# Performance work log

Hardware: AMD Instinct MI355X
Metric: run time of the kernel (lower is better)

## Reference

```python
import jax, jax.numpy as jnp
import numpy as np

N_NODES = 50000
N_EDGES = 800000
IN, HID, OUT = 128, 128, 64


def gcn_layer(x, W, b, src, dst, n):
    """PyG GCNConv: add self-loops, symmetric normalization, linear, scatter-add, bias."""
    loop = jnp.arange(n, dtype=src.dtype)
    s = jnp.concatenate([src, loop])  # message sources
    d = jnp.concatenate([dst, loop])  # message destinations
    deg = jax.ops.segment_sum(jnp.ones(s.shape[0], dtype=x.dtype), d, num_segments=n)
    dinv = jnp.where(deg > 0, jax.lax.rsqrt(deg), jnp.zeros_like(deg))
    norm = dinv[s] * dinv[d]  # [E+N]
    h = x @ W                 # dense transform first (PyG order)
    agg = jax.ops.segment_sum(h[s] * norm[:, None], d, num_segments=n)  # [N, out]
    return agg + b


def setup_inputs() -> dict:
    key = jax.random.key(0)
    ks = jax.random.split(key, 8)
    x = jax.random.normal(ks[0], (N_NODES, IN), dtype=jnp.float32)
    edge_index = jax.random.randint(ks[1], (2, N_EDGES), 0, N_NODES, dtype=jnp.int32)
    s = 0.05
    W1 = jax.random.normal(ks[2], (IN, HID), dtype=jnp.float32) * s
    b1 = jnp.zeros((HID,), dtype=jnp.float32)
    W2 = jax.random.normal(ks[3], (HID, HID), dtype=jnp.float32) * s
    b2 = jnp.zeros((HID,), dtype=jnp.float32)
    W3 = jax.random.normal(ks[4], (HID, OUT), dtype=jnp.float32) * s
    b3 = jnp.zeros((OUT,), dtype=jnp.float32)
    return {"x": x, "edge_index": edge_index, "W1": W1, "b1": b1,
            "W2": W2, "b2": b2, "W3": W3, "b3": b3}


def reference(x, edge_index, W1, b1, W2, b2, W3, b3):
    src, dst = edge_index[0], edge_index[1]
    n = x.shape[0]
    # dropout is identity in eval mode; ReLU follows every layer (incl. last) as in source
    h = jax.nn.relu(gcn_layer(x, W1, b1, src, dst, n))
    h = jax.nn.relu(gcn_layer(h, W2, b2, src, dst, n))
    h = jax.nn.relu(gcn_layer(h, W3, b3, src, dst, n))
    return jax.nn.log_softmax(h, axis=1)
```

## Files before the change

### kernel.cpp

```cpp
#include <hip/hip_runtime.h>
#include <math.h>


typedef __attribute__((ext_vector_type(8))) short short8;
typedef __attribute__((ext_vector_type(4))) float f32x4;

#define PADROW 50115
#define CAP 64
#define NPART 8

__device__ inline unsigned short f2bf(float x) {
    unsigned int u = __float_as_uint(x);
    u += 0x7fffu + ((u >> 16) & 1u);
    return (unsigned short)(u >> 16);
}
__device__ inline float blo(unsigned int v) { return __uint_as_float(v << 16); }
__device__ inline float bhi(unsigned int v) { return __uint_as_float(v & 0xffff0000u); }


__global__ void prep0_kernel(int* __restrict__ deg, int N,
                             unsigned int* __restrict__ col32, int colw,
                             const float* __restrict__ W1, unsigned short* __restrict__ W1t,
                             const float* __restrict__ W2, unsigned short* __restrict__ W2t,
                             const float* __restrict__ W3, unsigned short* __restrict__ W3t,
                             unsigned short* __restrict__ hbuf) {
    int i = blockIdx.x * blockDim.x + threadIdx.x;
    if (i < N) deg[i] = 0;
    if (i < colw) col32[i] = 0xC3C3C3C3u;
    if (i < 16384) {
        int k = i >> 7, n = i & 127;
        W1t[(size_t)n * 128 + k] = f2bf(W1[i]);
    } else if (i < 32768) {
        int j = i - 16384;
        int k = j >> 7, n = j & 127;
        W2t[(size_t)n * 128 + k] = f2bf(W2[j]);
    } else if (i < 40960) {
        int j = i - 32768;
        int k = j >> 6, n = j & 63;
        W3t[(size_t)n * 128 + k] = f2bf(W3[j]);
    }
    if (i < 16)
        ((uint4*)(hbuf + (size_t)PADROW * 128))[i] = make_uint4(0, 0, 0, 0);
}

__global__ void build_ell_kernel(const int* __restrict__ src, const int* __restrict__ dst,
                                 int* __restrict__ deg, unsigned short* __restrict__ col_ell,
                                 int E, int N, int nblk_per_part) {
    int part = blockIdx.x & (NPART - 1);
    int blk  = blockIdx.x / NPART;
    int npr = (N + NPART - 1) / NPART;
    int lo = part * npr;
    int hi = min(N, lo + npr);
    int stride = nblk_per_part * blockDim.x;
    for (int e = blk * blockDim.x + threadIdx.x; e < E; e += stride) {
        int d = dst[e];
        if (d >= lo && d < hi) {
            int rk = atomicAdd(&deg[d], 1);
            if (rk < CAP) col_ell[(size_t)d * CAP + rk] = (unsigned short)src[e];
        }
    }
}

template<int H, bool AF32>
__global__ __launch_bounds__(256) void gemm_mfma(const void* __restrict__ Av,
                                                 const unsigned short* __restrict__ Wt,
                                                 const int* __restrict__ deg,
                                                 unsigned short* __restrict__ C, int M) {
    __shared__ __attribute__((aligned(16))) unsigned short As[128][136];
    __shared__ __attribute__((aligned(16))) unsigned short Ws[H][136];
    int tid = threadIdx.x;
    int row0 = blockIdx.x * 128;
    if (AF32) {
        const float* A = (const float*)Av;
        #pragma unroll
        for (int g = tid; g < 128 * 32; g += 256) {
            int r = g >> 5, c = g & 31;
            int gr = row0 + r;
            ushort4 o = make_ushort4(0, 0, 0, 0);
            if (gr < M) {
                float4 v = *(const float4*)(A + (size_t)gr * 128 + c * 4);
                o.x = f2bf(v.x); o.y = f2bf(v.y); o.z = f2bf(v.z); o.w = f2bf(v.w);
            }
            *(ushort4*)&As[r][c * 4] = o;
        }
    } else {
        const unsigned short* A = (const unsigned short*)Av;
        #pragma unroll
        for (int g = tid; g < 128 * 16; g += 256) {
            int r = g >> 4, c = g & 15;
            int gr = row0 + r;
            uint4 v = make_uint4(0, 0, 0, 0);
            if (gr < M) v = *(const uint4*)(A + (size_t)gr * 128 + c * 8);
            *(uint4*)&As[r][c * 8] = v;
        }
    }
    #pragma unroll
    for (int g = tid; g < H * 16; g += 256) {
        int r = g >> 4, c = g & 15;
        *(uint4*)&Ws[r][c * 8] = *(const uint4*)(Wt + (size_t)r * 128 + c * 8);
    }
    if (H == 64 && blockIdx.x == 0 && tid < 8)
        ((uint4*)(C + (size_t)PADROW * 64))[tid] = make_uint4(0, 0, 0, 0);
    __syncthreads();

    int wave = tid >> 6, lane = tid & 63;
    int lr = lane & 15;
    int lk = (lane >> 4) * 8;

    short8 af[2][4];
    float dv[2][4];
    #pragma unroll
    for (int t = 0; t < 2; ++t) {
        int base = wave * 32 + t * 16;
        #pragma unroll
        for (int ks = 0; ks < 4; ++ks)
            af[t][ks] = *(const short8*)&As[base + lr][ks * 32 + lk];
        #pragma unroll
        for (int r = 0; r < 4; ++r) {
            int grow = row0 + base + (lane >> 4) * 4 + r;
            dv[t][r] = (grow < M) ? rsqrtf((float)deg[grow] + 1.0f) : 0.0f;
        }
    }

    #pragma unroll
    for (int ct = 0; ct < H / 16; ++ct) {
        f32x4 acc0 = {0.f, 0.f, 0.f, 0.f};
        f32x4 acc1 = {0.f, 0.f, 0.f, 0.f};
        #pragma unroll
        for (int ks = 0; ks < 4; ++ks) {
            short8 wf = *(const short8*)&Ws[ct * 16 + lr][ks * 32 + lk];
            acc0 = __builtin_amdgcn_mfma_f32_16x16x32_bf16(af[0][ks], wf, acc0, 0, 0, 0);
            acc1 = __builtin_amdgcn_mfma_f32_16x16x32_bf16(af[1][ks], wf, acc1, 0, 0, 0);
        }
        int gcol = ct * 16 + lr;
        #pragma unroll
        for (int r = 0; r < 4; ++r) {
            int g0 = row0 + wave * 32 + (lane >> 4) * 4 + r;
            if (g0 < M) C[(size_t)g0 * H + gcol] = f2bf(acc0[r] * dv[0][r]);
            int g1 = g0 + 16;
            if (g1 < M) C[(size_t)g1 * H + gcol] = f2bf(acc1[r] * dv[1][r]);
        }
    }
}

__global__ __launch_bounds__(256, 4) void spmm128_kernel(const uint2* __restrict__ h2,
                                                         const unsigned short* __restrict__ col_ell,
                                                         const int* __restrict__ deg,
                                                         const float* __restrict__ bias,
                                                         uint2* __restrict__ out2, int N) {
    int wid = blockIdx.x * 8 + (threadIdx.x >> 5);
    int c = threadIdx.x & 31;
    if (wid >= N) return;
    const uint4* cell4 = (const uint4*)(col_ell + (size_t)wid * CAP);
    int dg = deg[wid];
    uint2 hv = h2[(size_t)wid * 32 + c];
    float a0 = blo(hv.x), a1 = bhi(hv.x), a2 = blo(hv.y), a3 = bhi(hv.y);
    {
        uint4 q0 = cell4[0], q1 = cell4[1], q2 = cell4[2];
        unsigned int cw[12] = {q0.x, q0.y, q0.z, q0.w, q1.x, q1.y, q1.z, q1.w,
                               q2.x, q2.y, q2.z, q2.w};
        uint2 g[24];
        #pragma unroll
        for (int u = 0; u < 12; ++u) {
            g[2 * u]     = h2[(size_t)(cw[u] & 0xffffu) * 32 + c];
            g[2 * u + 1] = h2[(size_t)(cw[u] >> 16) * 32 + c];
        }
        #pragma unroll
        for (int u = 0; u < 24; ++u) {
            a0 += blo(g[u].x); a1 += bhi(g[u].x);
            a2 += blo(g[u].y); a3 += bhi(g[u].y);
        }
    }
    if (dg > 24) {
        uint4 q0 = cell4[3], q1 = cell4[4], q2 = cell4[5];
        unsigned int cw[12] = {q0.x, q0.y, q0.z, q0.w, q1.x, q1.y, q1.z, q1.w,
                               q2.x, q2.y, q2.z, q2.w};
        uint2 g[24];
        #pragma unroll
        for (int u = 0; u < 12; ++u) {
            g[2 * u]     = h2[(size_t)(cw[u] & 0xffffu) * 32 + c];
            g[2 * u + 1] = h2[(size_t)(cw[u] >> 16) * 32 + c];
        }
        #pragma unroll
        for (int u = 0; u < 24; ++u) {
            a0 += blo(g[u].x); a1 += bhi(g[u].x);
            a2 += blo(g[u].y); a3 += bhi(g[u].y);
        }
        if (dg > 48) {
            uint4 q0 = cell4[6], q1 = cell4[7];
            unsigned int cw[8] = {q0.x, q0.y, q0.z, q0.w, q1.x, q1.y, q1.z, q1.w};
            uint2 g[16];
            #pragma unroll
            for (int u = 0; u < 8; ++u) {
                g[2 * u]     = h2[(size_t)(cw[u] & 0xffffu) * 32 + c];
                g[2 * u + 1] = h2[(size_t)(cw[u] >> 16) * 32 + c];
            }
            #pragma unroll
            for (int u = 0; u < 16; ++u) {
                a0 += blo(g[u].x); a1 += bhi(g[u].x);
                a2 += blo(g[u].y); a3 += bhi(g[u].y);
            }
        }
    }
    float dv = rsqrtf((float)dg + 1.0f);
    float4 b4 = ((const float4*)bias)[c];
    a0 = fmaxf(fmaf(a0, dv, b4.x), 0.0f);
    a1 = fmaxf(fmaf(a1, dv, b4.y), 0.0f);
    a2 = fmaxf(fmaf(a2, dv, b4.z), 0.0f);
    a3 = fmaxf(fmaf(a3, dv, b4.w), 0.0f);
    uint2 o;
    o.x = (unsigned int)f2bf(a0) | ((unsigned int)f2bf(a1) << 16);
    o.y = (unsigned int)f2bf(a2) | ((unsigned int)f2bf(a3) << 16);
    out2[(size_t)wid * 32 + c] = o;
}

__global__ __launch_bounds__(256, 4) void spmm64_lsm_kernel(const unsigned int* __restrict__ h1,
                                                            const unsigned short* __restrict__ col_ell,
                                                            const int* __restrict__ deg,
                                                            const float* __restrict__ bias,
                                                            float2* __restrict__ out2, int N) {
    int wid = blockIdx.x * 8 + (threadIdx.x >> 5);
    int c = threadIdx.x & 31;
    if (wid >= N) return;
    const uint4* cell4 = (const uint4*)(col_ell + (size_t)wid * CAP);
    int dg = deg[wid];
    unsigned int hv = h1[(size_t)wid * 32 + c];
    float a0 = blo(hv), a1 = bhi(hv);
    {
        uint4 q0 = cell4[0], q1 = cell4[1], q2 = cell4[2];
        unsigned int cw[12] = {q0.x, q0.y, q0.z, q0.w, q1.x, q1.y, q1.z, q1.w,
                               q2.x, q2.y, q2.z, q2.w};
        unsigned int g[24];
        #pragma unroll
        for (int u = 0; u < 12; ++u) {
            g[2 * u]     = h1[(size_t)(cw[u] & 0xffffu) * 32 + c];
            g[2 * u + 1] = h1[(size_t)(cw[u] >> 16) * 32 + c];
        }
        #pragma unroll
        for (int u = 0; u < 24; ++u) { a0 += blo(g[u]); a1 += bhi(g[u]); }
    }
    if (dg > 24) {
        uint4 q0 = cell4[3], q1 = cell4[4], q2 = cell4[5];
        unsigned int cw[12] = {q0.x, q0.y, q0.z, q0.w, q1.x, q1.y, q1.z, q1.w,
                               q2.x, q2.y, q2.z, q2.w};
        unsigned int g[24];
        #pragma unroll
        for (int u = 0; u < 12; ++u) {
            g[2 * u]     = h1[(size_t)(cw[u] & 0xffffu) * 32 + c];
            g[2 * u + 1] = h1[(size_t)(cw[u] >> 16) * 32 + c];
        }
        #pragma unroll
        for (int u = 0; u < 24; ++u) { a0 += blo(g[u]); a1 += bhi(g[u]); }
        if (dg > 48) {
            uint4 q0 = cell4[6], q1 = cell4[7];
            unsigned int cw[8] = {q0.x, q0.y, q0.z, q0.w, q1.x, q1.y, q1.z, q1.w};
            unsigned int g[16];
            #pragma unroll
            for (int u = 0; u < 8; ++u) {
                g[2 * u]     = h1[(size_t)(cw[u] & 0xffffu) * 32 + c];
                g[2 * u + 1] = h1[(size_t)(cw[u] >> 16) * 32 + c];
            }
            #pragma unroll
            for (int u = 0; u < 16; ++u) { a0 += blo(g[u]); a1 += bhi(g[u]); }
        }
    }
    float dv = rsqrtf((float)dg + 1.0f);
    float2 b2 = ((const float2*)bias)[c];
    a0 = fmaxf(fmaf(a0, dv, b2.x), 0.0f);
    a1 = fmaxf(fmaf(a1, dv, b2.y), 0.0f);
    float m = fmaxf(a0, a1);
    #pragma unroll
    for (int off = 16; off; off >>= 1) m = fmaxf(m, __shfl_xor(m, off));
    float ssum = expf(a0 - m) + expf(a1 - m);
    #pragma unroll
    for (int off = 16; off; off >>= 1) ssum += __shfl_xor(ssum, off);
    float lse = m + logf(ssum);
    float2 o;
    o.x = a0 - lse;
    o.y = a1 - lse;
    out2[(size_t)wid * 32 + c] = o;
}


extern "C" void kernel_launch(void* const* d_in, const int* in_sizes, int n_in,
                              void* d_out, int out_size, void* d_ws, size_t ws_size,
                              hipStream_t stream) {
    const float* x  = (const float*)d_in[0];
    const int*   ei = (const int*)d_in[1];
    const float* W1 = (const float*)d_in[2];
    const float* b1 = (const float*)d_in[3];
    const float* W2 = (const float*)d_in[4];
    const float* b2 = (const float*)d_in[5];
    const float* W3 = (const float*)d_in[6];
    const float* b3 = (const float*)d_in[7];
    float* out = (float*)d_out;

    const int IN = 128, HID = 128, OUT = 64;
    int N = in_sizes[0] / IN;
    int E = in_sizes[1] / 2;
    const int* srcp = ei;
    const int* dstp = ei + E;

    char* p = (char*)d_ws;
    auto alloc = [&](size_t bytes) {
        char* r = p;
        p += (bytes + 255) & ~(size_t)255;
        return r;
    };
    int* deg = (int*)alloc((size_t)N * 4);
    unsigned short* col_ell = (unsigned short*)alloc((size_t)N * CAP * 2);
    unsigned short* W1t  = (unsigned short*)alloc((size_t)IN * HID * 2);
    unsigned short* W2t  = (unsigned short*)alloc((size_t)HID * HID * 2);
    unsigned short* W3t  = (unsigned short*)alloc((size_t)HID * OUT * 2);
    unsigned short* hbuf = (unsigned short*)alloc((size_t)(PADROW + 1) * HID * 2);
    unsigned short* abuf = (unsigned short*)alloc((size_t)N * HID * 2);

    int colw = N * CAP / 2;
    int prep0_grid = (max(colw, 40960) + 255) / 256;
    prep0_kernel<<<prep0_grid, 256, 0, stream>>>(deg, N, (unsigned int*)col_ell, colw,
                                                 W1, W1t, W2, W2t, W3, W3t, hbuf);
    int nblk_per_part = 512;
    build_ell_kernel<<<NPART * nblk_per_part, 256, 0, stream>>>(srcp, dstp, deg, col_ell,
                                                                E, N, nblk_per_part);

    int spmm_blocks = (N + 7) / 8;
    int gemm_blocks = (N + 127) / 128;

    gemm_mfma<128, true><<<gemm_blocks, 256, 0, stream>>>(x, W1t, deg, hbuf, N);
    spmm128_kernel<<<spmm_blocks, 256, 0, stream>>>((const uint2*)hbuf, col_ell, deg,
                                                    b1, (uint2*)abuf, N);
    gemm_mfma<128, false><<<gemm_blocks, 256, 0, stream>>>(abuf, W2t, deg, hbuf, N);
    spmm128_kernel<<<spmm_blocks, 256, 0, stream>>>((const uint2*)hbuf, col_ell, deg,
                                                    b2, (uint2*)abuf, N);
    gemm_mfma<64, false><<<gemm_blocks, 256, 0, stream>>>(abuf, W3t, deg, hbuf, N);
    spmm64_lsm_kernel<<<spmm_blocks, 256, 0, stream>>>((const unsigned int*)hbuf, col_ell, deg,
                                                       b3, (float2*)out, N);
}
```

Measured before the change: 161.9 us.

## Store 128-wide hidden features in column slices for cache-local SpMM gathers

Changes the 128-wide hidden buffers from row-major to eight 16-column slices, each laid out as [node][16]. GEMM outputs and inputs are rewritten to match, and a new SpMM kernel handles one slice per block, with 8 lanes per node and a degree-bounded loop. Each slice (~1.6MB) can stay in cache while its neighbour rows are gathered at random, which targets gather misses. In exchange it makes 8x more passes over the ELL index reads, issues narrower 4-byte gathers, and the strided GEMM stores and loads may coalesce less well.

```diff
diff --git a/kernel.cpp b/kernel.cpp
--- a/kernel.cpp
+++ b/kernel.cpp
@@ -6,6 +6,7 @@
 typedef __attribute__((ext_vector_type(4))) float f32x4;
 
 #define PADROW 50115
+#define NRH    (PADROW + 1)
 #define CAP 64
 #define NPART 8
 
@@ -23,7 +24,8 @@
                              const float* __restrict__ W1, unsigned short* __restrict__ W1t,
                              const float* __restrict__ W2, unsigned short* __restrict__ W2t,
                              const float* __restrict__ W3, unsigned short* __restrict__ W3t,
-                             unsigned short* __restrict__ hbuf) {
+                             unsigned short* __restrict__ hbuf,
+                             unsigned short* __restrict__ abuf) {
     int i = blockIdx.x * blockDim.x + threadIdx.x;
     if (i < N) deg[i] = 0;
     if (i < colw) col32[i] = 0xC3C3C3C3u;
@@ -39,8 +41,11 @@
         int k = j >> 6, n = j & 63;
         W3t[(size_t)n * 128 + k] = f2bf(W3[j]);
     }
-    if (i < 16)
-        ((uint4*)(hbuf + (size_t)PADROW * 128))[i] = make_uint4(0, 0, 0, 0);
+    if (i < 16) {
+        int s = i >> 1, part = i & 1;
+        ((uint4*)(hbuf + ((size_t)s * NRH + PADROW) * 16))[part] = make_uint4(0, 0, 0, 0);
+        ((uint4*)(abuf + ((size_t)s * NRH + PADROW) * 16))[part] = make_uint4(0, 0, 0, 0);
+    }
 }
 
 __global__ void build_ell_kernel(const int* __restrict__ src, const int* __restrict__ dst,
@@ -61,7 +66,7 @@
     }
 }
 
-template<int H, bool AF32>
+template<int H, bool AF32, bool ASLICE>
 __global__ __launch_bounds__(256) void gemm_mfma(const void* __restrict__ Av,
                                                  const unsigned short* __restrict__ Wt,
                                                  const int* __restrict__ deg,
@@ -90,7 +95,14 @@
             int r = g >> 4, c = g & 15;
             int gr = row0 + r;
             uint4 v = make_uint4(0, 0, 0, 0);
-            if (gr < M) v = *(const uint4*)(A + (size_t)gr * 128 + c * 8);
+            if (gr < M) {
+                if (ASLICE) {
+                    int sl = c >> 1, half = c & 1;
+                    v = *(const uint4*)(A + ((size_t)sl * NRH + gr) * 16 + half * 8);
+                } else {
+                    v = *(const uint4*)(A + (size_t)gr * 128 + c * 8);
+                }
+            }
             *(uint4*)&As[r][c * 8] = v;
         }
     }
@@ -132,86 +144,67 @@
             acc0 = __builtin_amdgcn_mfma_f32_16x16x32_bf16(af[0][ks], wf, acc0, 0, 0, 0);
             acc1 = __builtin_amdgcn_mfma_f32_16x16x32_bf16(af[1][ks], wf, acc1, 0, 0, 0);
         }
-        int gcol = ct * 16 + lr;
         #pragma unroll
         for (int r = 0; r < 4; ++r) {
             int g0 = row0 + wave * 32 + (lane >> 4) * 4 + r;
-            if (g0 < M) C[(size_t)g0 * H + gcol] = f2bf(acc0[r] * dv[0][r]);
             int g1 = g0 + 16;
-            if (g1 < M) C[(size_t)g1 * H + gcol] = f2bf(acc1[r] * dv[1][r]);
-        }
-    }
-}
-
-__global__ __launch_bounds__(256, 4) void spmm128_kernel(const uint2* __restrict__ h2,
-                                                         const unsigned short* __restrict__ col_ell,
-                                                         const int* __restrict__ deg,
-                                                         const float* __restrict__ bias,
-                                                         uint2* __restrict__ out2, int N) {
-    int wid = blockIdx.x * 8 + (threadIdx.x >> 5);
-    int c = threadIdx.x & 31;
-    if (wid >= N) return;
-    const uint4* cell4 = (const uint4*)(col_ell + (size_t)wid * CAP);
-    int dg = deg[wid];
-    uint2 hv = h2[(size_t)wid * 32 + c];
-    float a0 = blo(hv.x), a1 = bhi(hv.x), a2 = blo(hv.y), a3 = bhi(hv.y);
-    {
-        uint4 q0 = cell4[0], q1 = cell4[1], q2 = cell4[2];
-        unsigned int cw[12] = {q0.x, q0.y, q0.z, q0.w, q1.x, q1.y, q1.z, q1.w,
-                               q2.x, q2.y, q2.z, q2.w};
-        uint2 g[24];
-        #pragma unroll
-        for (int u = 0; u < 12; ++u) {
-            g[2 * u]     = h2[(size_t)(cw[u] & 0xffffu) * 32 + c];
-            g[2 * u + 1] = h2[(size_t)(cw[u] >> 16) * 32 + c];
-        }
-        #pragma unroll
-        for (int u = 0; u < 24; ++u) {
-            a0 += blo(g[u].x); a1 += bhi(g[u].x);
-            a2 += blo(g[u].y); a3 += bhi(g[u].y);
-        }
-    }
-    if (dg > 24) {
-        uint4 q0 = cell4[3], q1 = cell4[4], q2 = cell4[5];
-        unsigned int cw[12] = {q0.x, q0.y, q0.z, q0.w, q1.x, q1.y, q1.z, q1.w,
-                               q2.x, q2.y, q2.z, q2.w};
-        uint2 g[24];
-        #pragma unroll
-        for (int u = 0; u < 12; ++u) {
-            g[2 * u]     = h2[(size_t)(cw[u] & 0xffffu) * 32 + c];
-            g[2 * u + 1] = h2[(size_t)(cw[u] >> 16) * 32 + c];
-        }
-        #pragma unroll
-        for (int u = 0; u < 24; ++u) {
-            a0 += blo(g[u].x); a1 += bhi(g[u].x);
-            a2 += blo(g[u].y); a3 += bhi(g[u].y);
-        }
-        if (dg > 48) {
-            uint4 q0 = cell4[6], q1 = cell4[7];
-            unsigned int cw[8] = {q0.x, q0.y, q0.z, q0.w, q1.x, q1.y, q1.z, q1.w};
-            uint2 g[16];
-            #pragma unroll
-            for (int u = 0; u < 8; ++u) {
-                g[2 * u]     = h2[(size_t)(cw[u] & 0xffffu) * 32 + c];
-                g[2 * u + 1] = h2[(size_t)(cw[u] >> 16) * 32 + c];
+            if (H == 128) {
+                if (g0 < M) C[((size_t)ct * NRH + g0) * 16 + lr] = f2bf(acc0[r] * dv[0][r]);
+                if (g1 < M) C[((size_t)ct * NRH + g1) * 16 + lr] = f2bf(acc1[r] * dv[1][r]);
+            } else {
+                int gcol = ct * 16 + lr;
+                if (g0 < M) C[(size_t)g0 * H + gcol] = f2bf(acc0[r] * dv[0][r]);
+                if (g1 < M) C[(size_t)g1 * H + gcol] = f2bf(acc1[r] * dv[1][r]);
             }
-            #pragma unroll
-            for (int u = 0; u < 16; ++u) {
-                a0 += blo(g[u].x); a1 += bhi(g[u].x);
-                a2 += blo(g[u].y); a3 += bhi(g[u].y);
-            }
-        }
+        }
+    }
+}
+
+__global__ __launch_bounds__(256, 4) void spmm128_slice_kernel(const unsigned int* __restrict__ hs,
+                                                               const unsigned short* __restrict__ col_ell,
+                                                               const int* __restrict__ deg,
+                                                               const float* __restrict__ bias,
+                                                               unsigned int* __restrict__ outs,
+                                                               int N) {
+    int sl = blockIdx.x & 7;
+    int nb = blockIdx.x >> 3;
+    int lane = threadIdx.x & 63;
+    int wave = threadIdx.x >> 6;
+    int node = nb * 32 + wave * 8 + (lane >> 3);
+    int c = lane & 7;
+    bool valid = node < N;
+    int node_c = valid ? node : 0;
+    const unsigned int* h = hs + (size_t)sl * NRH * 8;
+    size_t base = (size_t)node_c * CAP;
+    int dg = valid ? deg[node_c] : 0;
+    unsigned int hv = h[(size_t)node_c * 8 + c];
+    float a0 = blo(hv), a1 = bhi(hv);
+    int mx = dg;
+    mx = max(mx, __shfl_xor(mx, 8));
+    mx = max(mx, __shfl_xor(mx, 16));
+    mx = max(mx, __shfl_xor(mx, 32));
+    #pragma unroll 1
+    for (int k0 = 0; k0 < CAP; k0 += 16) {
+        if (k0 > 0 && k0 >= mx) break;
+        uint4 q0 = *(const uint4*)(col_ell + base + k0);
+        uint4 q1 = *(const uint4*)(col_ell + base + k0 + 8);
+        unsigned int cw[8] = {q0.x, q0.y, q0.z, q0.w, q1.x, q1.y, q1.z, q1.w};
+        unsigned int g[16];
+        #pragma unroll
+        for (int u = 0; u < 8; ++u) {
+            g[2 * u]     = h[(size_t)(cw[u] & 0xffffu) * 8 + c];
+            g[2 * u + 1] = h[(size_t)(cw[u] >> 16) * 8 + c];
+        }
+        #pragma unroll
+        for (int u = 0; u < 16; ++u) { a0 += blo(g[u]); a1 += bhi(g[u]); }
     }
     float dv = rsqrtf((float)dg + 1.0f);
-    float4 b4 = ((const float4*)bias)[c];
-    a0 = fmaxf(fmaf(a0, dv, b4.x), 0.0f);
-    a1 = fmaxf(fmaf(a1, dv, b4.y), 0.0f);
-    a2 = fmaxf(fmaf(a2, dv, b4.z), 0.0f);
-    a3 = fmaxf(fmaf(a3, dv, b4.w), 0.0f);
-    uint2 o;
-    o.x = (unsigned int)f2bf(a0) | ((unsigned int)f2bf(a1) << 16);
-    o.y = (unsigned int)f2bf(a2) | ((unsigned int)f2bf(a3) << 16);
-    out2[(size_t)wid * 32 + c] = o;
+    float2 b2 = ((const float2*)bias)[sl * 8 + c];
+    a0 = fmaxf(fmaf(a0, dv, b2.x), 0.0f);
+    a1 = fmaxf(fmaf(a1, dv, b2.y), 0.0f);
+    if (valid)
+        outs[((size_t)sl * NRH + node) * 8 + c] =
+            (unsigned int)f2bf(a0) | ((unsigned int)f2bf(a1) << 16);
 }
 
 __global__ __launch_bounds__(256, 4) void spmm64_lsm_kernel(const unsigned int* __restrict__ h1,
@@ -312,27 +305,28 @@
     unsigned short* W1t  = (unsigned short*)alloc((size_t)IN * HID * 2);
     unsigned short* W2t  = (unsigned short*)alloc((size_t)HID * HID * 2);
     unsigned short* W3t  = (unsigned short*)alloc((size_t)HID * OUT * 2);
-    unsigned short* hbuf = (unsigned short*)alloc((size_t)(PADROW + 1) * HID * 2);
-    unsigned short* abuf = (unsigned short*)alloc((size_t)N * HID * 2);
+    unsigned short* hbuf = (unsigned short*)alloc((size_t)8 * NRH * 16 * 2);
+    unsigned short* abuf = (unsigned short*)alloc((size_t)8 * NRH * 16 * 2);
 
     int colw = N * CAP / 2;
     int prep0_grid = (max(colw, 40960) + 255) / 256;
     prep0_kernel<<<prep0_grid, 256, 0, stream>>>(deg, N, (unsigned int*)col_ell, colw,
-                                                 W1, W1t, W2, W2t, W3, W3t, hbuf);
+                                                 W1, W1t, W2, W2t, W3, W3t, hbuf, abuf);
     int nblk_per_part = 512;
     build_ell_kernel<<<NPART * nblk_per_part, 256, 0, stream>>>(srcp, dstp, deg, col_ell,
                                                                 E, N, nblk_per_part);
 
-    int spmm_blocks = (N + 7) / 8;
+    int slice_blocks = 8 * ((N + 31) / 32);
+    int spmm64_blocks = (N + 7) / 8;
     int gemm_blocks = (N + 127) / 128;
 
-    gemm_mfma<128, true><<<gemm_blocks, 256, 0, stream>>>(x, W1t, deg, hbuf, N);
-    spmm128_kernel<<<spmm_blocks, 256, 0, stream>>>((const uint2*)hbuf, col_ell, deg,
-                                                    b1, (uint2*)abuf, N);
-    gemm_mfma<128, false><<<gemm_blocks, 256, 0, stream>>>(abuf, W2t, deg, hbuf, N);
-    spmm128_kernel<<<spmm_blocks, 256, 0, stream>>>((const uint2*)hbuf, col_ell, deg,
-                                                    b2, (uint2*)abuf, N);
-    gemm_mfma<64, false><<<gemm_blocks, 256, 0, stream>>>(abuf, W3t, deg, hbuf, N);
-    spmm64_lsm_kernel<<<spmm_blocks, 256, 0, stream>>>((const unsigned int*)hbuf, col_ell, deg,
-                                                       b3, (float2*)out, N);
-}
+    gemm_mfma<128, true, false><<<gemm_blocks, 256, 0, stream>>>(x, W1t, deg, hbuf, N);
+    spmm128_slice_kernel<<<slice_blocks, 256, 0, stream>>>((const unsigned int*)hbuf, col_ell,
+                                                           deg, b1, (unsigned int*)abuf, N);
+    gemm_mfma<128, false, true><<<gemm_blocks, 256, 0, stream>>>(abuf, W2t, deg, hbuf, N);
+    spmm128_slice_kernel<<<slice_blocks, 256, 0, stream>>>((const unsigned int*)hbuf, col_ell,
+                                                           deg, b2, (unsigned int*)abuf, N);
+    gemm_mfma<64, false, true><<<gemm_blocks, 256, 0, stream>>>(abuf, W3t, deg, hbuf, N);
+    spmm64_lsm_kernel<<<spmm64_blocks, 256, 0, stream>>>((const unsigned int*)hbuf, col_ell, deg,
+                                                         b3, (float2*)out, N);
+}
```

Result: slower. 180.7 us (+11.7%).
